# Optimization experiments

Measured on AMD Instinct MI355X. Metric: run time of the kernel, lower is better.

The kernel has to match this reference:

```python
import math
import jax, jax.numpy as jnp
import numpy as np

B, L, D = 2, 2048, 512
H, DK, RANK, NH = 8, 64, 32, 1
K_MAX = 64
BANDWIDTH = 8.0
N_BUCKETS = 16


def setup_inputs() -> dict:
    key = jax.random.key(0)
    ks = jax.random.split(key, 14)
    s = 0.02
    return {
        "query": jax.random.normal(ks[0], (B, L, D), jnp.float32),
        "key": jax.random.normal(ks[1], (B, L, D), jnp.float32),
        "value": jax.random.normal(ks[2], (B, L, D), jnp.float32),
        "Wq": jax.random.normal(ks[3], (D, H * DK), jnp.float32) * s,
        "bq": jnp.zeros((H * DK,), jnp.float32),
        "Wk": jax.random.normal(ks[4], (D, H * DK), jnp.float32) * s,
        "bk": jnp.zeros((H * DK,), jnp.float32),
        "Wv": jax.random.normal(ks[5], (D, H * DK), jnp.float32) * s,
        "bv": jnp.zeros((H * DK,), jnp.float32),
        "U": jax.random.normal(ks[6], (H, DK, RANK), jnp.float32) * s,
        "V": jax.random.normal(ks[7], (H, RANK, D), jnp.float32) * s,
        "rv": jax.random.normal(ks[8], (H, DK, NH), jnp.float32),  # LSH random vectors (buffer)
        "Wo": jax.random.normal(ks[9], (H * D, D), jnp.float32) * s,
        "bo": jnp.zeros((D,), jnp.float32),
    }


def _lsh_hash(x, r):
    # binary quantize then bucketed floor hash: [B,L,dk] @ [dk,nh] -> [B,L,nh]
    xb = (x > 0).astype(x.dtype)
    return jnp.floor((xb @ r) / BANDWIDTH) % N_BUCKETS


def reference(query, key, value, Wq, bq, Wk, bk, Wv, bv, U, V, rv, Wo, bo):
    Bq, Lq, Dm = query.shape
    nheads, dk = U.shape[0], U.shape[1]
    q = (query @ Wq + bq).reshape(Bq, Lq, nheads, dk).transpose(0, 2, 1, 3)  # [B,H,L,dk]
    k = (key @ Wk + bk).reshape(Bq, Lq, nheads, dk).transpose(0, 2, 1, 3)
    v = (value @ Wv + bv).reshape(Bq, Lq, nheads, dk).transpose(0, 2, 1, 3)
    scale = math.sqrt(dk)  # optimized_sqrt(d_key), d_key power of two

    head_outputs = []
    for h in range(nheads):
        qh, kh, vh = q[:, h], k[:, h], v[:, h]  # [B,L,dk]
        qhash = _lsh_hash(qh, rv[h])  # [B,L,nh]
        khash = _lsh_hash(kh, rv[h])
        # [B,L,L] candidate match matrix (all hashes equal)
        matches = (qhash[:, :, None, :] == khash[:, None, :, :]).all(-1)
        # first K_MAX matching key indices in ascending order (== torch nonzero order)
        order = jnp.argsort(jnp.logical_not(matches), axis=-1, stable=True)
        cand = order[:, :, :K_MAX]  # [B,L,k_max]
        valid = jnp.take_along_axis(matches, cand, axis=-1)  # [B,L,k_max]
        ckeys = jnp.take_along_axis(kh[:, None, :, :], cand[..., None], axis=2)  # [B,L,k_max,dk]
        cvals = jnp.take_along_axis(vh[:, None, :, :], cand[..., None], axis=2)
        sim = jnp.einsum('bld,blkd->blk', qh, ckeys) / scale
        sim = jnp.where(valid, sim, -jnp.inf)
        attn = jax.nn.softmax(sim, axis=-1)  # invalid slots get exactly 0 weight
        # attention-weighted sum then low-rank up-projection (linear, so commutes
        # with the weighted sum; avoids the [B,L,k_max,d_model] intermediate)
        ctx = jnp.einsum('blk,blkd->bld', attn, cvals)  # [B,L,dk]
        head_outputs.append((ctx @ U[h]) @ V[h])  # [B,L,d_model]

    concat = jnp.concatenate(head_outputs, axis=-1)  # [B,L,H*d_model]
    return concat @ Wo + bo
```

## Files before the change

### kernel.cpp

```cpp
#include <hip/hip_runtime.h>
#include <math.h>

#define Bb 2
#define Ll 2048
#define Dd 512
#define Hh 8
#define DKq 64
#define NBUCK 16
#define KMAX 64
#define MAX_ITEMS 1280

__global__ __launch_bounds__(128) void proj_kernel(
    const float* __restrict__ Xq, const float* __restrict__ Xk, const float* __restrict__ Xv,
    const float* __restrict__ Wq, const float* __restrict__ Wk, const float* __restrict__ Wv,
    const float* __restrict__ bq, const float* __restrict__ bk, const float* __restrict__ bv,
    float* __restrict__ qb, float* __restrict__ kb, float* __restrict__ vb)
{
  const float *X, *W, *bias; float* dst;
  if (blockIdx.z == 0)      { X=Xq; W=Wq; bias=bq; dst=qb; }
  else if (blockIdx.z == 1) { X=Xk; W=Wk; bias=bk; dst=kb; }
  else                      { X=Xv; W=Wv; bias=bv; dst=vb; }
  __shared__ float As[32][68];
  __shared__ float Bs[32][132];
  const int tid = threadIdx.x;
  const int m0 = blockIdx.y * 64;
  const int n0 = blockIdx.x * 128;
  const int tx = tid & 15, ty = tid >> 4;

  float4 ar[4], br[8];
  #pragma unroll
  for (int i = 0; i < 4; i++) {
    int g = i * 128 + tid, row = g >> 3, c4 = g & 7;
    ar[i] = *(const float4*)&X[(size_t)(m0 + row) * 512 + c4 * 4];
  }
  #pragma unroll
  for (int i = 0; i < 8; i++) {
    int g = i * 128 + tid, row = g >> 5, c4 = g & 31;
    br[i] = *(const float4*)&W[(size_t)row * 512 + n0 + c4 * 4];
  }

  float acc[8][8] = {};
  for (int k0 = 0; k0 < 512; k0 += 32) {
    __syncthreads();
    #pragma unroll
    for (int i = 0; i < 4; i++) {
      int g = i * 128 + tid, row = g >> 3, c4 = g & 7;
      int mswz = ((c4 >> 1) & 1) << 3;
      As[c4*4+0][(row ^ mswz)] = ar[i].x;
      As[c4*4+1][(row ^ mswz)] = ar[i].y;
      As[c4*4+2][(row ^ mswz)] = ar[i].z;
      As[c4*4+3][(row ^ mswz)] = ar[i].w;
    }
    #pragma unroll
    for (int i = 0; i < 8; i++) {
      int g = i * 128 + tid, row = g >> 5, c4 = g & 31;
      *(float4*)&Bs[row][c4*4] = br[i];
    }
    __syncthreads();
    if (k0 + 32 < 512) {
      #pragma unroll
      for (int i = 0; i < 4; i++) {
        int g = i * 128 + tid, row = g >> 3, c4 = g & 7;
        ar[i] = *(const float4*)&X[(size_t)(m0 + row) * 512 + (k0 + 32) + c4 * 4];
      }
      #pragma unroll
      for (int i = 0; i < 8; i++) {
        int g = i * 128 + tid, row = g >> 5, c4 = g & 31;
        br[i] = *(const float4*)&W[(size_t)(k0 + 32 + row) * 512 + n0 + c4 * 4];
      }
    }
    #pragma unroll
    for (int kk = 0; kk < 32; kk++) {
      const int mswz = ((kk >> 3) & 1) << 3;
      const int mb = (ty * 8) ^ mswz;
      float4 a0 = *(const float4*)&As[kk][mb];
      float4 a1 = *(const float4*)&As[kk][mb + 4];
      float4 b0 = *(const float4*)&Bs[kk][tx*4];
      float4 b1 = *(const float4*)&Bs[kk][64 + tx*4];
      float av[8] = {a0.x,a0.y,a0.z,a0.w,a1.x,a1.y,a1.z,a1.w};
      float bw[8] = {b0.x,b0.y,b0.z,b0.w,b1.x,b1.y,b1.z,b1.w};
      #pragma unroll
      for (int i=0;i<8;i++)
        #pragma unroll
        for (int j=0;j<8;j++) acc[i][j] += av[i]*bw[j];
    }
  }
  const int head0 = n0 >> 6;
  const int d0 = tx * 4;
  #pragma unroll
  for (int i=0;i<8;i++) {
    int m = m0 + ty*8 + i;
    int b = m >> 11, l = m & 2047;
    float* drow0 = &dst[(((size_t)b*Hh + head0)*Ll + l)*DKq];
    float* drow1 = &dst[(((size_t)b*Hh + head0 + 1)*Ll + l)*DKq];
    #pragma unroll
    for (int j=0;j<4;j++) drow0[d0 + j] = acc[i][j]   + bias[n0 + tx*4 + j];
    #pragma unroll
    for (int j=0;j<4;j++) drow1[d0 + j] = acc[i][4+j] + bias[n0 + 64 + tx*4 + j];
  }
}

__global__ __launch_bounds__(256) void hash_kernel(
    const float* __restrict__ qb, const float* __restrict__ kb,
    const float* __restrict__ rv, int* __restrict__ qhash, int* __restrict__ khash)
{
  int gwave = (blockIdx.x * blockDim.x + threadIdx.x) >> 6;
  int lane = threadIdx.x & 63;
  const int NR = Bb * Hh * Ll;
  if (gwave >= 2 * NR) return;
  int isK = gwave >= NR;
  int row = isK ? gwave - NR : gwave;
  int h = (row >> 11) & 7;
  const float* src = isK ? kb : qb;
  float x = src[(size_t)row * DKq + lane];
  float r = rv[h * DKq + lane];
  float v = (x > 0.0f) ? r : 0.0f;
  #pragma unroll
  for (int off = 32; off; off >>= 1) v += __shfl_xor(v, off);
  if (lane == 0) {
    float fb = floorf(v * 0.125f);
    int ib = (int)fb;
    int bucket = ib & 15;
    (isK ? khash : qhash)[row] = bucket;
  }
}

__global__ __launch_bounds__(64) void kcand_kernel(
    const int* __restrict__ khash, int* __restrict__ kcand, int* __restrict__ kcount)
{
  int bh = blockIdx.x >> 4;
  int bucket = blockIdx.x & 15;
  int lane = threadIdx.x;
  const int* kh = &khash[bh * Ll];
  int* cl = &kcand[(size_t)blockIdx.x * KMAX];
  int total = 0;
  for (int c0 = 0; c0 < Ll && total < KMAX; c0 += 64) {
    int hv = kh[c0 + lane];
    unsigned long long m = __ballot(hv == bucket);
    int pre = __popcll(m & ((1ULL << lane) - 1ULL));
    if (hv == bucket && total + pre < KMAX) cl[total + pre] = c0 + lane;
    total += __popcll(m);
  }
  if (lane == 0) kcount[blockIdx.x] = total < KMAX ? total : KMAX;
}

__global__ __launch_bounds__(256) void qlist_kernel(
    const int* __restrict__ qhash, int* __restrict__ qoff, int* __restrict__ qlist)
{
  int bh = blockIdx.x;
  __shared__ int cnt[NBUCK], cur[NBUCK], off[NBUCK + 1];
  if (threadIdx.x < NBUCK) cnt[threadIdx.x] = 0;
  __syncthreads();
  const int* qh = &qhash[bh * Ll];
  for (int l = threadIdx.x; l < Ll; l += 256) atomicAdd(&cnt[qh[l]], 1);
  __syncthreads();
  if (threadIdx.x == 0) {
    int s = 0;
    for (int i = 0; i < NBUCK; i++) { off[i] = s; cur[i] = s; s += cnt[i]; }
    off[NBUCK] = s;
  }
  __syncthreads();
  if (threadIdx.x < NBUCK + 1) qoff[bh * (NBUCK + 1) + threadIdx.x] = off[threadIdx.x];
  for (int l = threadIdx.x; l < Ll; l += 256) {
    int p = atomicAdd(&cur[qh[l]], 1);
    qlist[bh * Ll + p] = l;
  }
}

__global__ __launch_bounds__(256) void worklist_kernel(
    const int* __restrict__ qoff, const int* __restrict__ kcount,
    int4* __restrict__ items, int* __restrict__ nitems)
{
  int t = threadIdx.x;
  int bh = t >> 4, bucket = t & 15;
  int o0 = qoff[bh * 17 + bucket], o1 = qoff[bh * 17 + bucket + 1];
  int cnt = kcount[t];
  int nq = o1 - o0;
  int n = (cnt > 0) ? ((nq + 31) >> 5) : 0;
  __shared__ int sc[256];
  sc[t] = n;
  __syncthreads();
  for (int off = 1; off < 256; off <<= 1) {
    int v = (t >= off) ? sc[t - off] : 0;
    __syncthreads();
    sc[t] += v;
    __syncthreads();
  }
  int start = sc[t] - n;
  for (int i = 0; i < n; i++) {
    int q0 = 32 * i;
    int qn = nq - q0; if (qn > 32) qn = 32;
    items[start + i] = make_int4(t, o0 + q0, qn, cnt);
  }
  if (t == 255) nitems[0] = sc[255];
}

__device__ __forceinline__ void lds_fence() {
  asm volatile("s_waitcnt lgkmcnt(0)" ::: "memory");
  __builtin_amdgcn_sched_barrier(0);
}

__global__ __launch_bounds__(256, 2) void attn_kernel(
    const float* __restrict__ qb, const float* __restrict__ kb, const float* __restrict__ vb,
    const int* __restrict__ qlist, const int* __restrict__ kcand,
    const int4* __restrict__ items, const int* __restrict__ nitems,
    float* __restrict__ ctx)
{
  __shared__ float qs_all[4][32 * 64];
  __shared__ float sa_all[4][64];
  const int wid = threadIdx.x >> 6, lane = threadIdx.x & 63;
  const int idx = blockIdx.x * 4 + wid;
  if (idx >= nitems[0]) return;
  const int4 it = items[idx];
  const int code = it.x, qstart = it.y, qn = it.z, cnt = it.w;
  const int bh = code >> 4;
  float* qs = qs_all[wid];
  float* sa = sa_all[wid];

  const float* qbh = qb + (size_t)bh * Ll * DKq;
  const float* kbh = kb + (size_t)bh * Ll * DKq;
  const float* vbh = vb + (size_t)bh * Ll * DKq;

  int qidx_v = (lane < qn)  ? qlist[bh * Ll + qstart + lane] : 0;
  int cidx_v = (lane < cnt) ? kcand[(size_t)code * KMAX + lane] : 0;

  float4 kr[16];
  {
    const float4* krow = (const float4*)kbh + (size_t)cidx_v * 16;
    #pragma unroll
    for (int i = 0; i < 16; i++) kr[i] = krow[i];
  }
  float vt[64];
  #pragma unroll
  for (int c = 0; c < 64; c++) {
    int rowc = __shfl(cidx_v, c);
    vt[c] = vbh[(size_t)rowc * DKq + lane];
  }
  #pragma unroll
  for (int i = 0; i < 8; i++) {
    int f = lane + 64 * i;
    int r = f >> 4, c4 = f & 15;
    int qrow = __shfl(qidx_v, r);
    float4 qv = *((const float4*)qbh + (size_t)qrow * 16 + c4);
    *(float4*)&qs[r * 64 + c4 * 4] = qv;
  }
  lds_fence();

  const int b = bh >> 3, h = bh & 7;
  const float4* qs4 = (const float4*)qs;
  const float4* sa4 = (const float4*)sa;

  for (int j = 0; j < qn; j++) {
    float s0 = 0.f, s1 = 0.f, s2 = 0.f, s3 = 0.f;
    #pragma unroll
    for (int i = 0; i < 16; i += 4) {
      float4 q0 = qs4[j * 16 + i + 0];
      float4 q1 = qs4[j * 16 + i + 1];
      float4 q2 = qs4[j * 16 + i + 2];
      float4 q3 = qs4[j * 16 + i + 3];
      s0 += q0.x*kr[i+0].x + q0.y*kr[i+0].y + q0.z*kr[i+0].z + q0.w*kr[i+0].w;
      s1 += q1.x*kr[i+1].x + q1.y*kr[i+1].y + q1.z*kr[i+1].z + q1.w*kr[i+1].w;
      s2 += q2.x*kr[i+2].x + q2.y*kr[i+2].y + q2.z*kr[i+2].z + q2.w*kr[i+2].w;
      s3 += q3.x*kr[i+3].x + q3.y*kr[i+3].y + q3.z*kr[i+3].z + q3.w*kr[i+3].w;
    }
    float s = ((s0 + s1) + (s2 + s3)) * 0.125f;
    s = (lane < cnt) ? s : -INFINITY;
    float m = s;
    #pragma unroll
    for (int off = 32; off; off >>= 1) m = fmaxf(m, __shfl_xor(m, off));
    float e = __expf(s - m);
    float sum = e;
    #pragma unroll
    for (int off = 32; off; off >>= 1) sum += __shfl_xor(sum, off);
    lds_fence();
    sa[lane] = e;
    lds_fence();
    float c0 = 0.f, c1 = 0.f, c2 = 0.f, c3 = 0.f;
    #pragma unroll
    for (int i = 0; i < 16; i++) {
      float4 a = sa4[i];
      c0 += a.x * vt[4*i + 0];
      c1 += a.y * vt[4*i + 1];
      c2 += a.z * vt[4*i + 2];
      c3 += a.w * vt[4*i + 3];
    }
    float ctxd = ((c0 + c1) + (c2 + c3)) / sum;
    int qrow = __shfl(qidx_v, j);
    ctx[((size_t)(b * Ll + qrow)) * 512 + h * 64 + lane] = ctxd;
  }
}

__global__ __launch_bounds__(256) void uv_kernel(
    const float* __restrict__ U, const float* __restrict__ V, float* __restrict__ T)
{
  int idx = blockIdx.x * 256 + threadIdx.x;
  int n = idx & 511, dk = (idx >> 9) & 63, h = idx >> 15;
  float acc = 0.f;
  #pragma unroll
  for (int r = 0; r < 32; r++)
    acc += U[((size_t)h * 64 + dk) * 32 + r] * V[((size_t)h * 32 + r) * 512 + n];
  T[idx] = acc;
}

__global__ __launch_bounds__(256) void m_kernel(
    const float* __restrict__ T, const float* __restrict__ Wo, float* __restrict__ Mf)
{
  __shared__ float Ts[16][68];
  __shared__ float Ws[16][68];
  const int h = blockIdx.y;
  const int n0 = blockIdx.x * 64;
  const int tid = threadIdx.x;
  const int tx = tid & 15, ty = tid >> 4;
  float acc[4][4] = {};
  for (int k0 = 0; k0 < 512; k0 += 16) {
    {
      int r = tid >> 2, cg = (tid & 3) << 2;
      float4 a = *(const float4*)&T[((size_t)(h*64 + r))*512 + k0 + cg];
      Ts[cg+0][r]=a.x; Ts[cg+1][r]=a.y; Ts[cg+2][r]=a.z; Ts[cg+3][r]=a.w;
    }
    {
      int row = tid >> 4, c4 = tid & 15;
      *(float4*)&Ws[row][c4*4] = *(const float4*)&Wo[((size_t)(h*512 + k0 + row))*512 + n0 + c4*4];
    }
    __syncthreads();
    #pragma unroll
    for (int kk = 0; kk < 16; kk++) {
      float4 a0 = *(const float4*)&Ts[kk][ty*4];
      float4 b0 = *(const float4*)&Ws[kk][tx*4];
      float av[4] = {a0.x,a0.y,a0.z,a0.w};
      float bw[4] = {b0.x,b0.y,b0.z,b0.w};
      #pragma unroll
      for (int i=0;i<4;i++)
        #pragma unroll
        for (int j=0;j<4;j++) acc[i][j] += av[i]*bw[j];
    }
    __syncthreads();
  }
  #pragma unroll
  for (int i=0;i<4;i++) {
    int row = h*64 + ty*4 + i;
    #pragma unroll
    for (int j=0;j<4;j++)
      Mf[(size_t)row * 512 + n0 + tx*4 + j] = acc[i][j];
  }
}

__global__ __launch_bounds__(128) void out_gemm(
    const float* __restrict__ A, const float* __restrict__ Bm,
    const float* __restrict__ bias, float* __restrict__ C)
{
  __shared__ float As[32][68];
  __shared__ float Bs[32][68];
  const int tid = threadIdx.x;
  const int m0 = blockIdx.y * 64, n0 = blockIdx.x * 64;
  const int tx = tid & 15, ty = tid >> 4;

  float4 ar[4], br[4];
  #pragma unroll
  for (int i = 0; i < 4; i++) {
    int g = i * 128 + tid, row = g >> 3, c4 = g & 7;
    ar[i] = *(const float4*)&A[(size_t)(m0 + row) * 512 + c4 * 4];
  }
  #pragma unroll
  for (int i = 0; i < 4; i++) {
    int g = i * 128 + tid, row = g >> 4, c4 = g & 15;
    br[i] = *(const float4*)&Bm[(size_t)row * 512 + n0 + c4 * 4];
  }

  float acc[8][4] = {};
  for (int k0 = 0; k0 < 512; k0 += 32) {
    __syncthreads();
    #pragma unroll
    for (int i = 0; i < 4; i++) {
      int g = i * 128 + tid, row = g >> 3, c4 = g & 7;
      int mswz = ((c4 >> 1) & 1) << 3;
      As[c4*4+0][(row ^ mswz)] = ar[i].x;
      As[c4*4+1][(row ^ mswz)] = ar[i].y;
      As[c4*4+2][(row ^ mswz)] = ar[i].z;
      As[c4*4+3][(row ^ mswz)] = ar[i].w;
    }
    #pragma unroll
    for (int i = 0; i < 4; i++) {
      int g = i * 128 + tid, row = g >> 4, c4 = g & 15;
      *(float4*)&Bs[row][c4*4] = br[i];
    }
    __syncthreads();
    if (k0 + 32 < 512) {
      #pragma unroll
      for (int i = 0; i < 4; i++) {
        int g = i * 128 + tid, row = g >> 3, c4 = g & 7;
        ar[i] = *(const float4*)&A[(size_t)(m0 + row) * 512 + (k0 + 32) + c4 * 4];
      }
      #pragma unroll
      for (int i = 0; i < 4; i++) {
        int g = i * 128 + tid, row = g >> 4, c4 = g & 15;
        br[i] = *(const float4*)&Bm[(size_t)(k0 + 32 + row) * 512 + n0 + c4 * 4];
      }
    }
    #pragma unroll
    for (int kk = 0; kk < 32; kk++) {
      const int mswz = ((kk >> 3) & 1) << 3;
      const int mb = (ty * 8) ^ mswz;
      float4 a0 = *(const float4*)&As[kk][mb];
      float4 a1 = *(const float4*)&As[kk][mb + 4];
      float4 b0 = *(const float4*)&Bs[kk][tx*4];
      float av[8] = {a0.x,a0.y,a0.z,a0.w,a1.x,a1.y,a1.z,a1.w};
      float bw[4] = {b0.x,b0.y,b0.z,b0.w};
      #pragma unroll
      for (int i=0;i<8;i++)
        #pragma unroll
        for (int j=0;j<4;j++) acc[i][j] += av[i]*bw[j];
    }
  }
  #pragma unroll
  for (int i=0;i<8;i++) {
    int m = m0 + ty*8 + i;
    #pragma unroll
    for (int j=0;j<4;j++) {
      int n = n0 + tx*4 + j;
      C[(size_t)m * 512 + n] = acc[i][j] + bias[n];
    }
  }
}

extern "C" void kernel_launch(void* const* d_in, const int* in_sizes, int n_in,
                              void* d_out, int out_size, void* d_ws, size_t ws_size,
                              hipStream_t stream)
{
  const float* query = (const float*)d_in[0];
  const float* key   = (const float*)d_in[1];
  const float* value = (const float*)d_in[2];
  const float* Wq = (const float*)d_in[3];
  const float* bq = (const float*)d_in[4];
  const float* Wk = (const float*)d_in[5];
  const float* bk = (const float*)d_in[6];
  const float* Wv = (const float*)d_in[7];
  const float* bv = (const float*)d_in[8];
  const float* U  = (const float*)d_in[9];
  const float* V  = (const float*)d_in[10];
  const float* rv = (const float*)d_in[11];
  const float* Wo = (const float*)d_in[12];
  const float* bo = (const float*)d_in[13];
  float* out = (float*)d_out;

  float* ws = (float*)d_ws;
  const size_t NQKV = (size_t)Bb * Hh * Ll * DKq;
  float* qb   = ws;
  float* kb   = qb + NQKV;
  float* vb   = kb + NQKV;
  float* ctx  = vb + NQKV;
  float* T    = ctx + NQKV;
  float* Mf   = T + (size_t)Hh * DKq * 512;
  int* qhash  = (int*)(Mf + 512 * 512);
  int* khash  = qhash + Bb * Hh * Ll;
  int* kcand  = khash + Bb * Hh * Ll;
  int* kcount = kcand + Bb * Hh * NBUCK * KMAX;
  int* qoff   = kcount + Bb * Hh * NBUCK;
  int* qlist  = qoff + Bb * Hh * (NBUCK + 1);
  int4* items = (int4*)(qlist + Bb * Hh * Ll);
  int* nitems = (int*)(items + MAX_ITEMS);

  proj_kernel<<<dim3(4, 64, 3), 128, 0, stream>>>(query, key, value,
                                                  Wq, Wk, Wv, bq, bk, bv,
                                                  qb, kb, vb);
  hash_kernel<<<(2 * Bb * Hh * Ll * 64) / 256, 256, 0, stream>>>(qb, kb, rv, qhash, khash);
  kcand_kernel<<<Bb * Hh * NBUCK, 64, 0, stream>>>(khash, kcand, kcount);
  qlist_kernel<<<Bb * Hh, 256, 0, stream>>>(qhash, qoff, qlist);
  worklist_kernel<<<1, 256, 0, stream>>>(qoff, kcount, items, nitems);
  attn_kernel<<<MAX_ITEMS / 4, 256, 0, stream>>>(qb, kb, vb, qlist, kcand,
                                                 items, nitems, ctx);
  uv_kernel<<<(Hh * DKq * 512) / 256, 256, 0, stream>>>(U, V, T);
  m_kernel<<<dim3(8, 8), 256, 0, stream>>>(T, Wo, Mf);
  out_gemm<<<dim3(8, 64), 128, 0, stream>>>(ctx, Mf, bo, out);
}
```

Measured before the change: 288.2 us.

## Use direct global-to-LDS async loads with double-buffered tiles in projection GEMM

The QKV projection GEMM now loads tiles with global_load_lds, which writes straight into shared memory, into two LDS buffers. The next tile's load is issued while the current one is computed. The A tile is stored row-major with an XOR swizzle instead of being transposed through registers. This removes the register staging and one barrier per iteration, at the cost of doubled LDS use and reliance on the builtin's completion semantics being covered by the single __syncthreads.

```diff
diff --git a/kernel.cpp b/kernel.cpp
--- a/kernel.cpp
+++ b/kernel.cpp
@@ -10,6 +10,12 @@
 #define KMAX 64
 #define MAX_ITEMS 1280
 
+__device__ __forceinline__ void gl_lds16(const float* g, float* l) {
+  __builtin_amdgcn_global_load_lds(
+      (const __attribute__((address_space(1))) void*)g,
+      (__attribute__((address_space(3))) void*)l, 16, 0, 0);
+}
+
 __global__ __launch_bounds__(128) void proj_kernel(
     const float* __restrict__ Xq, const float* __restrict__ Xk, const float* __restrict__ Xv,
     const float* __restrict__ Wq, const float* __restrict__ Wk, const float* __restrict__ Wv,
@@ -20,83 +26,81 @@
   if (blockIdx.z == 0)      { X=Xq; W=Wq; bias=bq; dst=qb; }
   else if (blockIdx.z == 1) { X=Xk; W=Wk; bias=bk; dst=kb; }
   else                      { X=Xv; W=Wv; bias=bv; dst=vb; }
-  __shared__ float As[32][68];
-  __shared__ float Bs[32][132];
+  __shared__ float As[2][64 * 32];
+  __shared__ float Bs[2][32 * 128];
   const int tid = threadIdx.x;
   const int m0 = blockIdx.y * 64;
   const int n0 = blockIdx.x * 128;
   const int tx = tid & 15, ty = tid >> 4;
-
-  float4 ar[4], br[8];
-  #pragma unroll
-  for (int i = 0; i < 4; i++) {
-    int g = i * 128 + tid, row = g >> 3, c4 = g & 7;
-    ar[i] = *(const float4*)&X[(size_t)(m0 + row) * 512 + c4 * 4];
-  }
-  #pragma unroll
-  for (int i = 0; i < 8; i++) {
-    int g = i * 128 + tid, row = g >> 5, c4 = g & 31;
-    br[i] = *(const float4*)&W[(size_t)row * 512 + n0 + c4 * 4];
-  }
+  const int lane = tid & 63, wid = tid >> 6;
+
+  const float* aSrc[4];
+  #pragma unroll
+  for (int j = 0; j < 4; j++) {
+    int jj = wid * 4 + j;
+    aSrc[j] = X + (size_t)(m0 + 8*jj + (lane >> 3)) * 512 + (((lane & 7) ^ jj) << 2);
+  }
+  const float* bSrc[8];
+  #pragma unroll
+  for (int j = 0; j < 8; j++) {
+    int jj = wid * 8 + j;
+    bSrc[j] = W + (size_t)(2*jj + (lane >> 5)) * 512 + n0 + ((lane & 31) << 2);
+  }
+
+  #pragma unroll
+  for (int j = 0; j < 4; j++) gl_lds16(aSrc[j],            &As[0][(wid*4+j)*256]);
+  #pragma unroll
+  for (int j = 0; j < 8; j++) gl_lds16(bSrc[j],            &Bs[0][(wid*8+j)*256]);
+  __syncthreads();
 
   float acc[8][8] = {};
-  for (int k0 = 0; k0 < 512; k0 += 32) {
-    __syncthreads();
-    #pragma unroll
-    for (int i = 0; i < 4; i++) {
-      int g = i * 128 + tid, row = g >> 3, c4 = g & 7;
-      int mswz = ((c4 >> 1) & 1) << 3;
-      As[c4*4+0][(row ^ mswz)] = ar[i].x;
-      As[c4*4+1][(row ^ mswz)] = ar[i].y;
-      As[c4*4+2][(row ^ mswz)] = ar[i].z;
-      As[c4*4+3][(row ^ mswz)] = ar[i].w;
-    }
-    #pragma unroll
-    for (int i = 0; i < 8; i++) {
-      int g = i * 128 + tid, row = g >> 5, c4 = g & 31;
-      *(float4*)&Bs[row][c4*4] = br[i];
-    }
-    __syncthreads();
-    if (k0 + 32 < 512) {
-      #pragma unroll
-      for (int i = 0; i < 4; i++) {
-        int g = i * 128 + tid, row = g >> 3, c4 = g & 7;
-        ar[i] = *(const float4*)&X[(size_t)(m0 + row) * 512 + (k0 + 32) + c4 * 4];
+  for (int t = 0; t < 16; t++) {
+    const int cur = t & 1;
+    if (t < 15) {
+      const int k0 = (t + 1) * 32;
+      #pragma unroll
+      for (int j = 0; j < 4; j++) gl_lds16(aSrc[j] + k0,              &As[cur^1][(wid*4+j)*256]);
+      #pragma unroll
+      for (int j = 0; j < 8; j++) gl_lds16(bSrc[j] + (size_t)k0*512,  &Bs[cur^1][(wid*8+j)*256]);
+    }
+    const float* Ac = &As[cur][0];
+    const float* Bc = &Bs[cur][0];
+    #pragma unroll
+    for (int kk4 = 0; kk4 < 8; kk4++) {
+      float4 a[8];
+      #pragma unroll
+      for (int i = 0; i < 8; i++)
+        a[i] = *(const float4*)&Ac[(ty*8 + i)*32 + ((kk4 ^ ty) << 2)];
+      #pragma unroll
+      for (int s = 0; s < 4; s++) {
+        const int kk = kk4*4 + s;
+        float4 b0 = *(const float4*)&Bc[kk*128 + tx*4];
+        float4 b1 = *(const float4*)&Bc[kk*128 + 64 + tx*4];
+        #pragma unroll
+        for (int i = 0; i < 8; i++) {
+          const float as = (s==0) ? a[i].x : (s==1) ? a[i].y : (s==2) ? a[i].z : a[i].w;
+          acc[i][0] += as * b0.x;  acc[i][1] += as * b0.y;
+          acc[i][2] += as * b0.z;  acc[i][3] += as * b0.w;
+          acc[i][4] += as * b1.x;  acc[i][5] += as * b1.y;
+          acc[i][6] += as * b1.z;  acc[i][7] += as * b1.w;
+        }
       }
-      #pragma unroll
-      for (int i = 0; i < 8; i++) {
-        int g = i * 128 + tid, row = g >> 5, c4 = g & 31;
-        br[i] = *(const float4*)&W[(size_t)(k0 + 32 + row) * 512 + n0 + c4 * 4];
-      }
-    }
-    #pragma unroll
-    for (int kk = 0; kk < 32; kk++) {
-      const int mswz = ((kk >> 3) & 1) << 3;
-      const int mb = (ty * 8) ^ mswz;
-      float4 a0 = *(const float4*)&As[kk][mb];
-      float4 a1 = *(const float4*)&As[kk][mb + 4];
-      float4 b0 = *(const float4*)&Bs[kk][tx*4];
-      float4 b1 = *(const float4*)&Bs[kk][64 + tx*4];
-      float av[8] = {a0.x,a0.y,a0.z,a0.w,a1.x,a1.y,a1.z,a1.w};
-      float bw[8] = {b0.x,b0.y,b0.z,b0.w,b1.x,b1.y,b1.z,b1.w};
-      #pragma unroll
-      for (int i=0;i<8;i++)
-        #pragma unroll
-        for (int j=0;j<8;j++) acc[i][j] += av[i]*bw[j];
-    }
-  }
+    }
+    __syncthreads();
+  }
+
   const int head0 = n0 >> 6;
   const int d0 = tx * 4;
   #pragma unroll
-  for (int i=0;i<8;i++) {
+  for (int i = 0; i < 8; i++) {
     int m = m0 + ty*8 + i;
     int b = m >> 11, l = m & 2047;
     float* drow0 = &dst[(((size_t)b*Hh + head0)*Ll + l)*DKq];
     float* drow1 = &dst[(((size_t)b*Hh + head0 + 1)*Ll + l)*DKq];
     #pragma unroll
-    for (int j=0;j<4;j++) drow0[d0 + j] = acc[i][j]   + bias[n0 + tx*4 + j];
-    #pragma unroll
-    for (int j=0;j<4;j++) drow1[d0 + j] = acc[i][4+j] + bias[n0 + 64 + tx*4 + j];
+    for (int j = 0; j < 4; j++) drow0[d0 + j] = acc[i][j]   + bias[n0 + tx*4 + j];
+    #pragma unroll
+    for (int j = 0; j < 4; j++) drow1[d0 + j] = acc[i][4+j] + bias[n0 + 64 + tx*4 + j];
   }
 }
 
```

Result: no change. 288.7 us (+0.2%).
